# Kernel tuning notes

Hardware: AMD Instinct MI355X
Metric: run time of the kernel (lower is better)

Reference implementation:

```python
import jax, jax.numpy as jnp
import numpy as np

B, K, D = 128, 2048, 512   # batch, out_features (classes), in_features
C = 1.0                    # curvature c


def setup_inputs() -> dict:
    key = jax.random.key(0)
    k1, k2, k3 = jax.random.split(key, 3)
    # inputs must lie strictly inside the Poincare ball of radius 1/sqrt(c)
    v = jax.random.normal(k1, (B, D), jnp.float32)
    inp = v * (0.7 / (1.0 + jnp.linalg.norm(v, axis=-1, keepdims=True)))
    # p is a hyperbolic parameter (init zeros in the module; use small in-ball
    # values here so the math is non-degenerate)
    pv = jax.random.normal(k2, (K, D), jnp.float32)
    p = pv * (0.3 / (1.0 + jnp.linalg.norm(pv, axis=-1, keepdims=True)))
    # a is Euclidean, xavier-uniform scale ~ 1/sqrt(D)
    a = jax.random.normal(k3, (K, D), jnp.float32) * (1.0 / np.sqrt(D))
    return {"inp": inp, "p": p, "a": a}


def hyperbolic_logits(inp, p, a, c):
    """Ganea et al. hyperbolic MLR logits.

    logit_k(x) = (lambda_{p_k} ||a_k|| / sqrt(c))
                 * asinh( 2 sqrt(c) <(-p_k) (+)_c x, a_k>
                          / ((1 - c ||(-p_k)(+)_c x||^2) ||a_k||) )
    """
    c = jnp.float32(c)
    sc = jnp.sqrt(c)
    u = -p                                   # [K,D]
    uv = jnp.einsum('bd,kd->bk', inp, u)     # <u_k, x_b>
    uu = jnp.sum(u * u, -1)                  # [K]
    vv = jnp.sum(inp * inp, -1)              # [B]
    # Mobius addition w = u (+)_c x, broadcast to [B,K,D]
    alpha = 1.0 + 2.0 * c * uv + c * vv[:, None]          # coeff of u
    beta = 1.0 - c * uu[None, :]                           # coeff of x
    den = 1.0 + 2.0 * c * uv + (c * c) * uu[None, :] * vv[:, None]
    w = (alpha[..., None] * u[None, :, :]
         + beta[..., None] * inp[:, None, :]) / den[..., None]   # [B,K,D]
    ww = jnp.sum(w * w, -1)                  # [B,K]
    wa = jnp.einsum('bkd,kd->bk', w, a)      # [B,K]
    a_norm = jnp.linalg.norm(a, axis=-1)     # [K]
    lam_p = 2.0 / (1.0 - c * jnp.sum(p * p, -1))   # conformal factor at p_k
    num = 2.0 * sc * wa
    denom = a_norm[None, :] * (1.0 - c * ww)
    return (lam_p * a_norm / sc)[None, :] * jnp.arcsinh(num / denom)  # [B,K]


def reference(inp, p, a):
    return hyperbolic_logits(inp, p, a, C)
```

## Files before the change

### kernel.cpp

```cpp
#include <hip/hip_runtime.h>
#include <hip/hip_bf16.h>

#define B_SZ 128
#define K_SZ 2048
#define D_SZ 512
#define ROWP 520

typedef __attribute__((ext_vector_type(8))) short short8;
typedef __attribute__((ext_vector_type(4))) float floatx4;

static __device__ inline unsigned short f2b(float f) {
  unsigned int u = __float_as_uint(f);
  return (unsigned short)((u + 0x7fffu + ((u >> 16) & 1u)) >> 16);
}

__global__ __launch_bounds__(256, 2) void fused_kernel(
    const float* __restrict__ x, const float* __restrict__ p,
    const float* __restrict__ a, float* __restrict__ out) {
  __shared__ unsigned short xs[32 * ROWP];
  __shared__ unsigned short ps[16 * ROWP];
  __shared__ unsigned short as_[16 * ROWP];
  __shared__ float stats[32 + 48];

  const int t = threadIdx.x;
  const int bm = (blockIdx.x >> 7) * 32;
  const int kn = (blockIdx.x & 127) * 16;

  {
    const int r = t >> 3, s = t & 7;
    const float4* src = (const float4*)(x + (size_t)(bm + r) * D_SZ);
    float vvp = 0.f;
#pragma unroll
    for (int i = 0; i < 16; ++i) {
      float4 v = src[s + i * 8];
      vvp += v.x * v.x + v.y * v.y + v.z * v.z + v.w * v.w;
      ushort4 c;
      c.x = f2b(v.x); c.y = f2b(v.y); c.z = f2b(v.z); c.w = f2b(v.w);
      *(ushort4*)&xs[r * ROWP + (s + i * 8) * 4] = c;
    }
    vvp += __shfl_xor(vvp, 1, 64);
    vvp += __shfl_xor(vvp, 2, 64);
    vvp += __shfl_xor(vvp, 4, 64);
    if (s == 0) stats[r] = vvp;
  }

  {
    const int r = t >> 4, s = t & 15;
    const float4* sp = (const float4*)(p + (size_t)(kn + r) * D_SZ);
    const float4* sa = (const float4*)(a + (size_t)(kn + r) * D_SZ);
    float pp = 0.f, pa = 0.f, aa = 0.f;
#pragma unroll
    for (int i = 0; i < 8; ++i) {
      float4 pv = sp[s + i * 16];
      float4 av = sa[s + i * 16];
      pp += pv.x * pv.x + pv.y * pv.y + pv.z * pv.z + pv.w * pv.w;
      pa += pv.x * av.x + pv.y * av.y + pv.z * av.z + pv.w * av.w;
      aa += av.x * av.x + av.y * av.y + av.z * av.z + av.w * av.w;
      ushort4 pc, ac;
      pc.x = f2b(pv.x); pc.y = f2b(pv.y); pc.z = f2b(pv.z); pc.w = f2b(pv.w);
      ac.x = f2b(av.x); ac.y = f2b(av.y); ac.z = f2b(av.z); ac.w = f2b(av.w);
      *(ushort4*)&ps[r * ROWP + (s + i * 16) * 4] = pc;
      *(ushort4*)&as_[r * ROWP + (s + i * 16) * 4] = ac;
    }
    pp += __shfl_xor(pp, 1, 64);
    pa += __shfl_xor(pa, 1, 64);
    aa += __shfl_xor(aa, 1, 64);
    pp += __shfl_xor(pp, 2, 64);
    pa += __shfl_xor(pa, 2, 64);
    aa += __shfl_xor(aa, 2, 64);
    pp += __shfl_xor(pp, 4, 64);
    pa += __shfl_xor(pa, 4, 64);
    aa += __shfl_xor(aa, 4, 64);
    pp += __shfl_xor(pp, 8, 64);
    pa += __shfl_xor(pa, 8, 64);
    aa += __shfl_xor(aa, 8, 64);
    if (s == 0) {
      stats[32 + r] = pp;
      stats[48 + r] = -pa;
      stats[64 + r] = sqrtf(aa);
    }
  }
  __syncthreads();

  const int w = t >> 6, lane = t & 63;
  const int row16 = lane & 15, quad = lane >> 4;
  const int wm = w & 1, dh = w >> 1;
  const unsigned short* xrow = &xs[(wm * 16 + row16) * ROWP + dh * 256 + quad * 8];
  const unsigned short* prow = &ps[row16 * ROWP + dh * 256 + quad * 8];
  const unsigned short* arow = &as_[row16 * ROWP + dh * 256 + quad * 8];
  floatx4 cs = {0.f, 0.f, 0.f, 0.f};
  floatx4 ca = {0.f, 0.f, 0.f, 0.f};
#pragma unroll
  for (int dc = 0; dc < 8; ++dc) {
    short8 af = *(const short8*)(xrow + dc * 32);
    short8 bp = *(const short8*)(prow + dc * 32);
    short8 bv = *(const short8*)(arow + dc * 32);
    cs = __builtin_amdgcn_mfma_f32_16x16x32_bf16(af, bp, cs, 0, 0, 0);
    ca = __builtin_amdgcn_mfma_f32_16x16x32_bf16(af, bv, ca, 0, 0, 0);
  }

  __syncthreads();
  float* part_s = (float*)ps;
  float* part_a = part_s + 1024;
  *(floatx4*)&part_s[(w * 64 + lane) * 4] = cs;
  *(floatx4*)&part_a[(w * 64 + lane) * 4] = ca;
  __syncthreads();

#pragma unroll
  for (int o = 0; o < 2; ++o) {
    const int idx = t + o * 256;
    const int m16 = idx >> 4;
    const int n = idx & 15;
    const int wmI = m16 >> 4, mr = m16 & 15;
    const int lsrc = ((mr >> 2) << 4) | n;
    const int reg = mr & 3;
    const float sdot = part_s[(wmI * 64 + lsrc) * 4 + reg] +
                       part_s[((2 + wmI) * 64 + lsrc) * 4 + reg];
    const float adot = part_a[(wmI * 64 + lsrc) * 4 + reg] +
                       part_a[((2 + wmI) * 64 + lsrc) * 4 + reg];
    const float vvb = stats[m16];
    const float uuk = stats[32 + n];
    const float nuak = stats[48 + n];
    const float ank = stats[64 + n];
    const float beta = 1.f - uuk;
    const float scale = (2.f / beta) * ank;
    const float uv = -sdot;
    const float alpha = 1.f + 2.f * uv + vvb;
    const float den = 1.f + 2.f * uv + uuk * vvb;
    const float inv = 1.f / den;
    const float wwn =
        (alpha * alpha * uuk + 2.f * alpha * beta * uv + beta * beta * vvb) *
        inv * inv;
    const float wa = (alpha * nuak + beta * adot) * inv;
    const float z = 2.f * wa / (ank * (1.f - wwn));
    out[(size_t)(bm + m16) * K_SZ + (kn + n)] = scale * asinhf(z);
  }
}

extern "C" void kernel_launch(void* const* d_in, const int* in_sizes, int n_in,
                              void* d_out, int out_size, void* d_ws, size_t ws_size,
                              hipStream_t stream) {
  const float* x = (const float*)d_in[0];
  const float* p = (const float*)d_in[1];
  const float* a = (const float*)d_in[2];
  float* out = (float*)d_out;
  (void)d_ws; (void)ws_size;

  fused_kernel<<<(B_SZ / 32) * (K_SZ / 16), 256, 0, stream>>>(x, p, a, out);
}
```

Baseline: 67.03 us.

## Shrink tile to 16 rows, feed p/a straight from global into MFMA registers

The block tile drops from 32x16 to 16x16 outputs, doubling the grid, and the four waves now split the D dimension four ways. The p and a rows are loaded from global memory straight into registers, converted to bf16 and fed to the MFMA without staging in shared memory. Their norms and cross products are reduced with shuffles and combined across waves in shared memory. This cuts LDS usage and allows higher occupancy, at the cost of re-reading p and a twice as often from global memory or L2.

```diff
diff --git a/kernel.cpp b/kernel.cpp
--- a/kernel.cpp
+++ b/kernel.cpp
@@ -14,127 +14,121 @@
   return (unsigned short)((u + 0x7fffu + ((u >> 16) & 1u)) >> 16);
 }
 
-__global__ __launch_bounds__(256, 2) void fused_kernel(
+__global__ __launch_bounds__(256, 4) void fused_kernel(
     const float* __restrict__ x, const float* __restrict__ p,
     const float* __restrict__ a, float* __restrict__ out) {
-  __shared__ unsigned short xs[32 * ROWP];
-  __shared__ unsigned short ps[16 * ROWP];
-  __shared__ unsigned short as_[16 * ROWP];
-  __shared__ float stats[32 + 48];
+  __shared__ unsigned short xs[16 * ROWP];
+  __shared__ float part_s[4 * 256];
+  __shared__ float part_a[4 * 256];
+  __shared__ float spp[4 * 16];
+  __shared__ float spa[4 * 16];
+  __shared__ float saa[4 * 16];
+  __shared__ float svv[16];
 
   const int t = threadIdx.x;
-  const int bm = (blockIdx.x >> 7) * 32;
+  const int lane = t & 63;
+  const int w = t >> 6;
+  const int row16 = lane & 15;
+  const int quad = lane >> 4;
+  const int bm = (blockIdx.x >> 7) * 16;
   const int kn = (blockIdx.x & 127) * 16;
+  const int d0 = w * 128;
 
   {
-    const int r = t >> 3, s = t & 7;
+    const int r = t >> 4, s = t & 15;
     const float4* src = (const float4*)(x + (size_t)(bm + r) * D_SZ);
     float vvp = 0.f;
 #pragma unroll
-    for (int i = 0; i < 16; ++i) {
-      float4 v = src[s + i * 8];
+    for (int i = 0; i < 8; ++i) {
+      float4 v = src[s + i * 16];
       vvp += v.x * v.x + v.y * v.y + v.z * v.z + v.w * v.w;
       ushort4 c;
       c.x = f2b(v.x); c.y = f2b(v.y); c.z = f2b(v.z); c.w = f2b(v.w);
-      *(ushort4*)&xs[r * ROWP + (s + i * 8) * 4] = c;
+      *(ushort4*)&xs[r * ROWP + (s + i * 16) * 4] = c;
     }
     vvp += __shfl_xor(vvp, 1, 64);
     vvp += __shfl_xor(vvp, 2, 64);
     vvp += __shfl_xor(vvp, 4, 64);
-    if (s == 0) stats[r] = vvp;
+    vvp += __shfl_xor(vvp, 8, 64);
+    if ((lane & 15) == 0) svv[t >> 4] = vvp;
   }
 
-  {
-    const int r = t >> 4, s = t & 15;
-    const float4* sp = (const float4*)(p + (size_t)(kn + r) * D_SZ);
-    const float4* sa = (const float4*)(a + (size_t)(kn + r) * D_SZ);
-    float pp = 0.f, pa = 0.f, aa = 0.f;
-#pragma unroll
-    for (int i = 0; i < 8; ++i) {
-      float4 pv = sp[s + i * 16];
-      float4 av = sa[s + i * 16];
-      pp += pv.x * pv.x + pv.y * pv.y + pv.z * pv.z + pv.w * pv.w;
-      pa += pv.x * av.x + pv.y * av.y + pv.z * av.z + pv.w * av.w;
-      aa += av.x * av.x + av.y * av.y + av.z * av.z + av.w * av.w;
-      ushort4 pc, ac;
-      pc.x = f2b(pv.x); pc.y = f2b(pv.y); pc.z = f2b(pv.z); pc.w = f2b(pv.w);
-      ac.x = f2b(av.x); ac.y = f2b(av.y); ac.z = f2b(av.z); ac.w = f2b(av.w);
-      *(ushort4*)&ps[r * ROWP + (s + i * 16) * 4] = pc;
-      *(ushort4*)&as_[r * ROWP + (s + i * 16) * 4] = ac;
-    }
-    pp += __shfl_xor(pp, 1, 64);
-    pa += __shfl_xor(pa, 1, 64);
-    aa += __shfl_xor(aa, 1, 64);
-    pp += __shfl_xor(pp, 2, 64);
-    pa += __shfl_xor(pa, 2, 64);
-    aa += __shfl_xor(aa, 2, 64);
-    pp += __shfl_xor(pp, 4, 64);
-    pa += __shfl_xor(pa, 4, 64);
-    aa += __shfl_xor(aa, 4, 64);
-    pp += __shfl_xor(pp, 8, 64);
-    pa += __shfl_xor(pa, 8, 64);
-    aa += __shfl_xor(aa, 8, 64);
-    if (s == 0) {
-      stats[32 + r] = pp;
-      stats[48 + r] = -pa;
-      stats[64 + r] = sqrtf(aa);
-    }
-  }
-  __syncthreads();
-
-  const int w = t >> 6, lane = t & 63;
-  const int row16 = lane & 15, quad = lane >> 4;
-  const int wm = w & 1, dh = w >> 1;
-  const unsigned short* xrow = &xs[(wm * 16 + row16) * ROWP + dh * 256 + quad * 8];
-  const unsigned short* prow = &ps[row16 * ROWP + dh * 256 + quad * 8];
-  const unsigned short* arow = &as_[row16 * ROWP + dh * 256 + quad * 8];
+  const float4* prow =
+      (const float4*)(p + (size_t)(kn + row16) * D_SZ + d0 + quad * 8);
+  const float4* arow =
+      (const float4*)(a + (size_t)(kn + row16) * D_SZ + d0 + quad * 8);
+  float pp = 0.f, pa = 0.f, aa = 0.f;
   floatx4 cs = {0.f, 0.f, 0.f, 0.f};
   floatx4 ca = {0.f, 0.f, 0.f, 0.f};
+  __syncthreads();
 #pragma unroll
-  for (int dc = 0; dc < 8; ++dc) {
-    short8 af = *(const short8*)(xrow + dc * 32);
-    short8 bp = *(const short8*)(prow + dc * 32);
-    short8 bv = *(const short8*)(arow + dc * 32);
+  for (int step = 0; step < 4; ++step) {
+    float4 p0 = prow[step * 8];
+    float4 p1 = prow[step * 8 + 1];
+    float4 a0 = arow[step * 8];
+    float4 a1 = arow[step * 8 + 1];
+    pp += p0.x * p0.x + p0.y * p0.y + p0.z * p0.z + p0.w * p0.w +
+          p1.x * p1.x + p1.y * p1.y + p1.z * p1.z + p1.w * p1.w;
+    aa += a0.x * a0.x + a0.y * a0.y + a0.z * a0.z + a0.w * a0.w +
+          a1.x * a1.x + a1.y * a1.y + a1.z * a1.z + a1.w * a1.w;
+    pa += p0.x * a0.x + p0.y * a0.y + p0.z * a0.z + p0.w * a0.w +
+          p1.x * a1.x + p1.y * a1.y + p1.z * a1.z + p1.w * a1.w;
+    short8 bp, bv;
+    bp[0] = (short)f2b(p0.x); bp[1] = (short)f2b(p0.y);
+    bp[2] = (short)f2b(p0.z); bp[3] = (short)f2b(p0.w);
+    bp[4] = (short)f2b(p1.x); bp[5] = (short)f2b(p1.y);
+    bp[6] = (short)f2b(p1.z); bp[7] = (short)f2b(p1.w);
+    bv[0] = (short)f2b(a0.x); bv[1] = (short)f2b(a0.y);
+    bv[2] = (short)f2b(a0.z); bv[3] = (short)f2b(a0.w);
+    bv[4] = (short)f2b(a1.x); bv[5] = (short)f2b(a1.y);
+    bv[6] = (short)f2b(a1.z); bv[7] = (short)f2b(a1.w);
+    short8 af =
+        *(const short8*)&xs[row16 * ROWP + d0 + step * 32 + quad * 8];
     cs = __builtin_amdgcn_mfma_f32_16x16x32_bf16(af, bp, cs, 0, 0, 0);
     ca = __builtin_amdgcn_mfma_f32_16x16x32_bf16(af, bv, ca, 0, 0, 0);
   }
 
-  __syncthreads();
-  float* part_s = (float*)ps;
-  float* part_a = part_s + 1024;
-  *(floatx4*)&part_s[(w * 64 + lane) * 4] = cs;
-  *(floatx4*)&part_a[(w * 64 + lane) * 4] = ca;
+  pp += __shfl_xor(pp, 16, 64); pp += __shfl_xor(pp, 32, 64);
+  pa += __shfl_xor(pa, 16, 64); pa += __shfl_xor(pa, 32, 64);
+  aa += __shfl_xor(aa, 16, 64); aa += __shfl_xor(aa, 32, 64);
+  if (quad == 0) {
+    spp[w * 16 + row16] = pp;
+    spa[w * 16 + row16] = pa;
+    saa[w * 16 + row16] = aa;
+  }
+  *(floatx4*)&part_s[t * 4] = cs;
+  *(floatx4*)&part_a[t * 4] = ca;
   __syncthreads();
 
+  const int m16 = t >> 4;
+  const int n = t & 15;
+  const int lsrc = ((m16 >> 2) << 4) | n;
+  const int reg = m16 & 3;
+  float sdot = 0.f, adot = 0.f;
+  float uuk = 0.f, pak = 0.f, aak = 0.f;
 #pragma unroll
-  for (int o = 0; o < 2; ++o) {
-    const int idx = t + o * 256;
-    const int m16 = idx >> 4;
-    const int n = idx & 15;
-    const int wmI = m16 >> 4, mr = m16 & 15;
-    const int lsrc = ((mr >> 2) << 4) | n;
-    const int reg = mr & 3;
-    const float sdot = part_s[(wmI * 64 + lsrc) * 4 + reg] +
-                       part_s[((2 + wmI) * 64 + lsrc) * 4 + reg];
-    const float adot = part_a[(wmI * 64 + lsrc) * 4 + reg] +
-                       part_a[((2 + wmI) * 64 + lsrc) * 4 + reg];
-    const float vvb = stats[m16];
-    const float uuk = stats[32 + n];
-    const float nuak = stats[48 + n];
-    const float ank = stats[64 + n];
-    const float beta = 1.f - uuk;
-    const float scale = (2.f / beta) * ank;
-    const float uv = -sdot;
-    const float alpha = 1.f + 2.f * uv + vvb;
-    const float den = 1.f + 2.f * uv + uuk * vvb;
-    const float inv = 1.f / den;
-    const float wwn =
-        (alpha * alpha * uuk + 2.f * alpha * beta * uv + beta * beta * vvb) *
-        inv * inv;
-    const float wa = (alpha * nuak + beta * adot) * inv;
-    const float z = 2.f * wa / (ank * (1.f - wwn));
-    out[(size_t)(bm + m16) * K_SZ + (kn + n)] = scale * asinhf(z);
+  for (int ww = 0; ww < 4; ++ww) {
+    sdot += part_s[(ww * 64 + lsrc) * 4 + reg];
+    adot += part_a[(ww * 64 + lsrc) * 4 + reg];
+    uuk += spp[ww * 16 + n];
+    pak += spa[ww * 16 + n];
+    aak += saa[ww * 16 + n];
   }
+  const float vvb = svv[m16];
+  const float nuak = -pak;
+  const float ank = sqrtf(aak);
+  const float beta = 1.f - uuk;
+  const float scale = (2.f / beta) * ank;
+  const float uv = -sdot;
+  const float alpha = 1.f + 2.f * uv + vvb;
+  const float den = 1.f + 2.f * uv + uuk * vvb;
+  const float inv = 1.f / den;
+  const float wwn =
+      (alpha * alpha * uuk + 2.f * alpha * beta * uv + beta * beta * vvb) *
+      inv * inv;
+  const float wa = (alpha * nuak + beta * adot) * inv;
+  const float z = 2.f * wa / (ank * (1.f - wwn));
+  out[(size_t)(bm + m16) * K_SZ + (kn + n)] = scale * asinhf(z);
 }
 
 extern "C" void kernel_launch(void* const* d_in, const int* in_sizes, int n_in,
@@ -146,5 +140,5 @@
   float* out = (float*)d_out;
   (void)d_ws; (void)ws_size;
 
-  fused_kernel<<<(B_SZ / 32) * (K_SZ / 16), 256, 0, stream>>>(x, p, a, out);
+  fused_kernel<<<(B_SZ / 16) * (K_SZ / 16), 256, 0, stream>>>(x, p, a, out);
 }
```

Result: slower. 70.98 us (+5.9%).

## Use 64-row batch tiles with full-D per wave and drop LDS split-K reduction

Applied to the files above, without the earlier changes.

Each block now covers 64 batch rows instead of 32, so the grid halves and every p/a tile is converted and reduced once per 64 rows rather than per 32. Each wave takes its own 16 rows over the full reduction dimension, which removes the cross-wave partial-sum exchange through shared memory and its two barriers; the epilogue reads the MFMA accumulators directly. Loads of p/a and output stores become nontemporal. The cost is a larger LDS footprint, launch bounds of one block per SM, and a longer serial MFMA chain per wave with fewer blocks for latency hiding.

```diff
diff --git a/kernel.cpp b/kernel.cpp
--- a/kernel.cpp
+++ b/kernel.cpp
@@ -14,84 +14,77 @@
   return (unsigned short)((u + 0x7fffu + ((u >> 16) & 1u)) >> 16);
 }
 
-__global__ __launch_bounds__(256, 2) void fused_kernel(
+__global__ __launch_bounds__(256, 1) void fused_kernel(
     const float* __restrict__ x, const float* __restrict__ p,
     const float* __restrict__ a, float* __restrict__ out) {
-  __shared__ unsigned short xs[32 * ROWP];
+  __shared__ unsigned short xs[64 * ROWP];
   __shared__ unsigned short ps[16 * ROWP];
   __shared__ unsigned short as_[16 * ROWP];
-  __shared__ float stats[32 + 48];
+  __shared__ float svv[64];
+  __shared__ float spp[16], spa[16], saa[16];
 
   const int t = threadIdx.x;
-  const int bm = (blockIdx.x >> 7) * 32;
+  const int lane = t & 63;
+  const int w = t >> 6;
+  const int row16 = lane & 15;
+  const int quad = lane >> 4;
+  const int bm = (blockIdx.x >> 7) * 64;
   const int kn = (blockIdx.x & 127) * 16;
 
   {
-    const int r = t >> 3, s = t & 7;
-    const float4* src = (const float4*)(x + (size_t)(bm + r) * D_SZ);
+    const int r = t >> 4, s = t & 15;
+    const floatx4* sp = (const floatx4*)(p + (size_t)(kn + r) * D_SZ);
+    const floatx4* sa = (const floatx4*)(a + (size_t)(kn + r) * D_SZ);
+    float pp = 0.f, pa = 0.f, aa = 0.f;
+#pragma unroll
+    for (int i = 0; i < 8; ++i) {
+      floatx4 pv = __builtin_nontemporal_load(&sp[s + i * 16]);
+      floatx4 av = __builtin_nontemporal_load(&sa[s + i * 16]);
+      pp += pv[0] * pv[0] + pv[1] * pv[1] + pv[2] * pv[2] + pv[3] * pv[3];
+      pa += pv[0] * av[0] + pv[1] * av[1] + pv[2] * av[2] + pv[3] * av[3];
+      aa += av[0] * av[0] + av[1] * av[1] + av[2] * av[2] + av[3] * av[3];
+      ushort4 pc, ac;
+      pc.x = f2b(pv[0]); pc.y = f2b(pv[1]); pc.z = f2b(pv[2]); pc.w = f2b(pv[3]);
+      ac.x = f2b(av[0]); ac.y = f2b(av[1]); ac.z = f2b(av[2]); ac.w = f2b(av[3]);
+      *(ushort4*)&ps[r * ROWP + (s + i * 16) * 4] = pc;
+      *(ushort4*)&as_[r * ROWP + (s + i * 16) * 4] = ac;
+    }
+    pp += __shfl_xor(pp, 1, 64); pa += __shfl_xor(pa, 1, 64);
+    aa += __shfl_xor(aa, 1, 64);
+    pp += __shfl_xor(pp, 2, 64); pa += __shfl_xor(pa, 2, 64);
+    aa += __shfl_xor(aa, 2, 64);
+    pp += __shfl_xor(pp, 4, 64); pa += __shfl_xor(pa, 4, 64);
+    aa += __shfl_xor(aa, 4, 64);
+    pp += __shfl_xor(pp, 8, 64); pa += __shfl_xor(pa, 8, 64);
+    aa += __shfl_xor(aa, 8, 64);
+    if (s == 0) { spp[r] = pp; spa[r] = pa; saa[r] = aa; }
+  }
+
+  {
+    const int r = t >> 2, s = t & 3;
+    const float4* sx = (const float4*)(x + (size_t)(bm + r) * D_SZ);
     float vvp = 0.f;
 #pragma unroll
-    for (int i = 0; i < 16; ++i) {
-      float4 v = src[s + i * 8];
+    for (int i = 0; i < 32; ++i) {
+      float4 v = sx[s + i * 4];
       vvp += v.x * v.x + v.y * v.y + v.z * v.z + v.w * v.w;
       ushort4 c;
       c.x = f2b(v.x); c.y = f2b(v.y); c.z = f2b(v.z); c.w = f2b(v.w);
-      *(ushort4*)&xs[r * ROWP + (s + i * 8) * 4] = c;
+      *(ushort4*)&xs[r * ROWP + (s + i * 4) * 4] = c;
     }
     vvp += __shfl_xor(vvp, 1, 64);
     vvp += __shfl_xor(vvp, 2, 64);
-    vvp += __shfl_xor(vvp, 4, 64);
-    if (s == 0) stats[r] = vvp;
-  }
-
-  {
-    const int r = t >> 4, s = t & 15;
-    const float4* sp = (const float4*)(p + (size_t)(kn + r) * D_SZ);
-    const float4* sa = (const float4*)(a + (size_t)(kn + r) * D_SZ);
-    float pp = 0.f, pa = 0.f, aa = 0.f;
-#pragma unroll
-    for (int i = 0; i < 8; ++i) {
-      float4 pv = sp[s + i * 16];
-      float4 av = sa[s + i * 16];
-      pp += pv.x * pv.x + pv.y * pv.y + pv.z * pv.z + pv.w * pv.w;
-      pa += pv.x * av.x + pv.y * av.y + pv.z * av.z + pv.w * av.w;
-      aa += av.x * av.x + av.y * av.y + av.z * av.z + av.w * av.w;
-      ushort4 pc, ac;
-      pc.x = f2b(pv.x); pc.y = f2b(pv.y); pc.z = f2b(pv.z); pc.w = f2b(pv.w);
-      ac.x = f2b(av.x); ac.y = f2b(av.y); ac.z = f2b(av.z); ac.w = f2b(av.w);
-      *(ushort4*)&ps[r * ROWP + (s + i * 16) * 4] = pc;
-      *(ushort4*)&as_[r * ROWP + (s + i * 16) * 4] = ac;
-    }
-    pp += __shfl_xor(pp, 1, 64);
-    pa += __shfl_xor(pa, 1, 64);
-    aa += __shfl_xor(aa, 1, 64);
-    pp += __shfl_xor(pp, 2, 64);
-    pa += __shfl_xor(pa, 2, 64);
-    aa += __shfl_xor(aa, 2, 64);
-    pp += __shfl_xor(pp, 4, 64);
-    pa += __shfl_xor(pa, 4, 64);
-    aa += __shfl_xor(aa, 4, 64);
-    pp += __shfl_xor(pp, 8, 64);
-    pa += __shfl_xor(pa, 8, 64);
-    aa += __shfl_xor(aa, 8, 64);
-    if (s == 0) {
-      stats[32 + r] = pp;
-      stats[48 + r] = -pa;
-      stats[64 + r] = sqrtf(aa);
-    }
+    if (s == 0) svv[r] = vvp;
   }
   __syncthreads();
 
-  const int w = t >> 6, lane = t & 63;
-  const int row16 = lane & 15, quad = lane >> 4;
-  const int wm = w & 1, dh = w >> 1;
-  const unsigned short* xrow = &xs[(wm * 16 + row16) * ROWP + dh * 256 + quad * 8];
-  const unsigned short* prow = &ps[row16 * ROWP + dh * 256 + quad * 8];
-  const unsigned short* arow = &as_[row16 * ROWP + dh * 256 + quad * 8];
+  const unsigned short* xrow = &xs[(w * 16 + row16) * ROWP + quad * 8];
+  const unsigned short* prow = &ps[row16 * ROWP + quad * 8];
+  const unsigned short* arow = &as_[row16 * ROWP + quad * 8];
   floatx4 cs = {0.f, 0.f, 0.f, 0.f};
   floatx4 ca = {0.f, 0.f, 0.f, 0.f};
 #pragma unroll
-  for (int dc = 0; dc < 8; ++dc) {
+  for (int dc = 0; dc < 16; ++dc) {
     short8 af = *(const short8*)(xrow + dc * 32);
     short8 bp = *(const short8*)(prow + dc * 32);
     short8 bv = *(const short8*)(arow + dc * 32);
@@ -99,41 +92,29 @@
     ca = __builtin_amdgcn_mfma_f32_16x16x32_bf16(af, bv, ca, 0, 0, 0);
   }
 
-  __syncthreads();
-  float* part_s = (float*)ps;
-  float* part_a = part_s + 1024;
-  *(floatx4*)&part_s[(w * 64 + lane) * 4] = cs;
-  *(floatx4*)&part_a[(w * 64 + lane) * 4] = ca;
-  __syncthreads();
-
+  const int n = row16;
+  const int k = kn + n;
+  const float uuk = spp[n];
+  const float nuak = -spa[n];
+  const float ank = sqrtf(saa[n]);
+  const float beta = 1.f - uuk;
+  const float scale = (2.f / beta) * ank;
 #pragma unroll
-  for (int o = 0; o < 2; ++o) {
-    const int idx = t + o * 256;
-    const int m16 = idx >> 4;
-    const int n = idx & 15;
-    const int wmI = m16 >> 4, mr = m16 & 15;
-    const int lsrc = ((mr >> 2) << 4) | n;
-    const int reg = mr & 3;
-    const float sdot = part_s[(wmI * 64 + lsrc) * 4 + reg] +
-                       part_s[((2 + wmI) * 64 + lsrc) * 4 + reg];
-    const float adot = part_a[(wmI * 64 + lsrc) * 4 + reg] +
-                       part_a[((2 + wmI) * 64 + lsrc) * 4 + reg];
-    const float vvb = stats[m16];
-    const float uuk = stats[32 + n];
-    const float nuak = stats[48 + n];
-    const float ank = stats[64 + n];
-    const float beta = 1.f - uuk;
-    const float scale = (2.f / beta) * ank;
-    const float uv = -sdot;
+  for (int r = 0; r < 4; ++r) {
+    const int m = w * 16 + quad * 4 + r;
+    const float vvb = svv[m];
+    const float uv = -cs[r];
+    const float xa = ca[r];
     const float alpha = 1.f + 2.f * uv + vvb;
     const float den = 1.f + 2.f * uv + uuk * vvb;
     const float inv = 1.f / den;
     const float wwn =
         (alpha * alpha * uuk + 2.f * alpha * beta * uv + beta * beta * vvb) *
         inv * inv;
-    const float wa = (alpha * nuak + beta * adot) * inv;
+    const float wa = (alpha * nuak + beta * xa) * inv;
     const float z = 2.f * wa / (ank * (1.f - wwn));
-    out[(size_t)(bm + m16) * K_SZ + (kn + n)] = scale * asinhf(z);
+    __builtin_nontemporal_store(scale * asinhf(z),
+                                &out[(size_t)(bm + m) * K_SZ + k]);
   }
 }
 
@@ -146,5 +127,5 @@
   float* out = (float*)d_out;
   (void)d_ws; (void)ws_size;
 
-  fused_kernel<<<(B_SZ / 32) * (K_SZ / 16), 256, 0, stream>>>(x, p, a, out);
+  fused_kernel<<<(B_SZ / 64) * (K_SZ / 16), 256, 0, stream>>>(x, p, a, out);
 }
```

After: 68.02 us. Within noise of the previous version (+1.5%).
